# Kernel tuning notes

Measured on AMD Instinct MI355X. Metric: run time of the kernel, lower is better.

Reference implementation:

```python
import jax, jax.numpy as jnp
import numpy as np

N, E, F_IN, HID, HEADS, G = 50000, 800000, 128, 32, 8, 64
NEG_SLOPE = 0.2  # PyG GATConv default leaky_relu slope


def gat_conv(x, src, dst, W, att_src, att_dst, bias, heads, out_ch):
    """PyG-style GATConv (concat=True, self-loops already included in src/dst)."""
    n = x.shape[0]
    h = (x @ W).reshape(n, heads, out_ch)            # [N,H,C]
    a_src = jnp.sum(h * att_src, axis=-1)            # [N,H]
    a_dst = jnp.sum(h * att_dst, axis=-1)            # [N,H]
    e = jax.nn.leaky_relu(a_src[src] + a_dst[dst], NEG_SLOPE)  # [Et,H]
    # segment softmax over incoming edges of each destination node
    m = jax.ops.segment_max(e, dst, num_segments=n)
    e = jnp.exp(e - m[dst])
    denom = jax.ops.segment_sum(e, dst, num_segments=n)
    alpha = e / (denom[dst] + 1e-16)                 # [Et,H]
    msg = h[src] * alpha[:, :, None]                 # [Et,H,C]
    out = jax.ops.segment_sum(msg, dst, num_segments=n)
    return out.reshape(n, heads * out_ch) + bias


def setup_inputs() -> dict:
    key = jax.random.key(0)
    ks = jax.random.split(key, 16)
    x = jax.random.normal(ks[0], (N, F_IN), dtype=jnp.float32)
    edge_index = jax.random.randint(ks[1], (2, E), 0, N, dtype=jnp.int64)
    batch = jnp.sort(jax.random.randint(ks[2], (N,), 0, G, dtype=jnp.int64))
    s = 0.05
    params = dict(
        W1=jax.random.normal(ks[3], (F_IN, HEADS * HID), jnp.float32) * s,
        att_src1=jax.random.normal(ks[4], (1, HEADS, HID), jnp.float32) * s,
        att_dst1=jax.random.normal(ks[5], (1, HEADS, HID), jnp.float32) * s,
        b1=jnp.zeros((HEADS * HID,), jnp.float32),
        W2=jax.random.normal(ks[6], (HEADS * HID, HID), jnp.float32) * s,
        att_src2=jax.random.normal(ks[7], (1, 1, HID), jnp.float32) * s,
        att_dst2=jax.random.normal(ks[8], (1, 1, HID), jnp.float32) * s,
        b2=jnp.zeros((HID,), jnp.float32),
        Wo=jax.random.normal(ks[9], (HID, 1), jnp.float32) * s,
        bo=jnp.zeros((1,), jnp.float32),
    )
    return dict(x=x, edge_index=edge_index, batch=batch, **params)


def reference(x, edge_index, batch, W1, att_src1, att_dst1, b1,
              W2, att_src2, att_dst2, b2, Wo, bo):
    # add self loops (PyG GATConv default add_self_loops=True)
    loop = jnp.arange(N, dtype=edge_index.dtype)
    src = jnp.concatenate([edge_index[0], loop])
    dst = jnp.concatenate([edge_index[1], loop])

    h = jax.nn.elu(gat_conv(x, src, dst, W1, att_src1, att_dst1, b1, HEADS, HID))
    # dropout p=0.2 is identity in eval mode
    h = jax.nn.elu(gat_conv(h, src, dst, W2, att_src2, att_dst2, b2, 1, HID))

    # global mean pool over graphs
    sums = jax.ops.segment_sum(h, batch, num_segments=G)          # [G,HID]
    cnts = jax.ops.segment_sum(jnp.ones((N,), h.dtype), batch, num_segments=G)
    pooled = sums / jnp.maximum(cnts, 1.0)[:, None]

    return jax.nn.sigmoid(pooled @ Wo + bo)                        # [G,1]
```

## Files before the change

### kernel.cpp

```cpp
#include <hip/hip_runtime.h>
#include <hip/hip_bf16.h>
#include <math.h>

#define NN 50000
#define NE 800000
#define ET (NE + NN)
#define FIN 128
#define HEADS 8
#define HID 32
#define C1 (HEADS * HID)
#define NG 64
#define NEG 0.2f

#define EPB 4096
#define NBKT 782
#define CAP 2048

typedef __attribute__((ext_vector_type(8))) unsigned short ushort8_t;
typedef __attribute__((ext_vector_type(4))) unsigned short ushort4_t;
typedef __attribute__((ext_vector_type(2))) float float2_t;
typedef __attribute__((ext_vector_type(8))) short bf16x8;
typedef __attribute__((ext_vector_type(4))) float f32x4;

__device__ __forceinline__ float lrelu(float v) { return v > 0.f ? v : NEG * v; }
__device__ __forceinline__ float elu1(float v)  { return v > 0.f ? v : expm1f(v); }
__device__ __forceinline__ unsigned short f2bf(float f) {
    __hip_bfloat16 b = __float2bfloat16(f);
    return *reinterpret_cast<unsigned short*>(&b);
}
__device__ __forceinline__ float bf2f(unsigned short u) {
    return __uint_as_float(((unsigned)u) << 16);
}
__device__ __forceinline__ void dec_fma16(uint4 r, float e, float2_t* acc) {
    float2_t ev = {e, e};
    acc[0] += ev * __builtin_amdgcn_cvt_pk_f32_fp8((int)r.x, false);
    acc[1] += ev * __builtin_amdgcn_cvt_pk_f32_fp8((int)r.x, true);
    acc[2] += ev * __builtin_amdgcn_cvt_pk_f32_fp8((int)r.y, false);
    acc[3] += ev * __builtin_amdgcn_cvt_pk_f32_fp8((int)r.y, true);
    acc[4] += ev * __builtin_amdgcn_cvt_pk_f32_fp8((int)r.z, false);
    acc[5] += ev * __builtin_amdgcn_cvt_pk_f32_fp8((int)r.z, true);
    acc[6] += ev * __builtin_amdgcn_cvt_pk_f32_fp8((int)r.w, false);
    acc[7] += ev * __builtin_amdgcn_cvt_pk_f32_fp8((int)r.w, true);
}

__global__ __launch_bounds__(256) void bkt_scatter_kernel(const int* __restrict__ ei,
                                                          int* __restrict__ bcur,
                                                          unsigned* __restrict__ bkt) {
    __shared__ unsigned ep[EPB];
    __shared__ int lh[NBKT];
    int t = threadIdx.x;
    int base = blockIdx.x * EPB;
    int nloc = ET - base; if (nloc > EPB) nloc = EPB;
    for (int i = t; i < NBKT; i += 256) lh[i] = 0;
    __syncthreads();
    for (int k = t; k < nloc; k += 256) {
        int i = base + k;
        int s, d;
        if (i < NE) { s = ei[i]; d = ei[NE + i]; }
        else        { s = i - NE; d = s; }
        ep[k] = (unsigned)s | ((unsigned)(d & 63) << 16) | ((unsigned)(d >> 6) << 22);
        atomicAdd(&lh[d >> 6], 1);
    }
    __syncthreads();
    for (int i = t; i < NBKT; i += 256) {
        int c = lh[i];
        lh[i] = c ? atomicAdd(&bcur[i], c) : 0;
    }
    __syncthreads();
    for (int k = t; k < nloc; k += 256) {
        unsigned v = ep[k];
        int b = (int)(v >> 22);
        int pos = atomicAdd(&lh[b], 1);
        if (pos < CAP) bkt[(size_t)b * CAP + pos] = v & 0x3FFFFFu;
    }
}

__global__ __launch_bounds__(256) void bkt_scan_kernel(const int* __restrict__ bcur,
                                                       int* __restrict__ bbase,
                                                       int* __restrict__ rowptr) {
    __shared__ int wsum[4];
    int t = threadIdx.x, lane = t & 63, w = t >> 6;
    int idx = t * 4;
    int a0 = (idx + 0 < NBKT) ? bcur[idx + 0] : 0;
    int a1 = (idx + 1 < NBKT) ? bcur[idx + 1] : 0;
    int a2 = (idx + 2 < NBKT) ? bcur[idx + 2] : 0;
    int a3 = (idx + 3 < NBKT) ? bcur[idx + 3] : 0;
    int v = a0 + a1 + a2 + a3;
    int inc = v;
    #pragma unroll
    for (int off = 1; off < 64; off <<= 1) {
        int u = __shfl_up(inc, off, 64);
        if (lane >= off) inc += u;
    }
    if (lane == 63) wsum[w] = inc;
    __syncthreads();
    int woff = 0;
    #pragma unroll
    for (int i = 0; i < 4; ++i) if (i < w) woff += wsum[i];
    int excl = woff + inc - v;
    if (idx + 0 < NBKT) bbase[idx + 0] = excl;
    if (idx + 1 < NBKT) bbase[idx + 1] = excl + a0;
    if (idx + 2 < NBKT) bbase[idx + 2] = excl + a0 + a1;
    if (idx + 3 < NBKT) bbase[idx + 3] = excl + a0 + a1 + a2;
    if (t == 255) rowptr[NN] = woff + inc;
}

__global__ __launch_bounds__(256) void csr_kernel(const unsigned* __restrict__ bkt,
                                                  const int* __restrict__ bcur,
                                                  const int* __restrict__ bbase,
                                                  int* __restrict__ rowptr,
                                                  int* __restrict__ ssrc) {
    __shared__ int nb[64];
    __shared__ int nc[64];
    int b = blockIdx.x, t = threadIdx.x;
    int cnt = bcur[b]; if (cnt > CAP) cnt = CAP;
    int gbase = bbase[b];
    if (t < 64) nc[t] = 0;
    __syncthreads();
    const unsigned* e = bkt + (size_t)b * CAP;
    for (int k = t; k < cnt; k += 256)
        atomicAdd(&nc[e[k] >> 16], 1);
    __syncthreads();
    if (t < 64) {
        int v = nc[t];
        int inc = v;
        #pragma unroll
        for (int off = 1; off < 64; off <<= 1) {
            int u = __shfl_up(inc, off, 64);
            if (t >= off) inc += u;
        }
        int start = gbase + inc - v;
        nb[t] = start;
        int node = b * 64 + t;
        if (node < NN) rowptr[node] = start;
    }
    __syncthreads();
    for (int k = t; k < cnt; k += 256) {
        unsigned v = e[k];
        int pos = atomicAdd(&nb[v >> 16], 1);
        ssrc[pos] = (int)(v & 0xFFFFu);
    }
}

__global__ __launch_bounds__(256) void cvt_w1_kernel(const float* __restrict__ W1,
                                                     unsigned short* __restrict__ w1swz) {
    int t = blockIdx.x * 256 + threadIdx.x;
    int fid = t >> 6, lane = t & 63;
    int tnt = fid >> 2, ks = fid & 3;
    int n = tnt * 16 + (lane & 15);
    int k0 = ks * 32 + (lane >> 4) * 8;
    ushort8_t o;
    #pragma unroll
    for (int j = 0; j < 8; ++j) o[j] = f2bf(W1[(k0 + j) * C1 + n]);
    *(ushort8_t*)&w1swz[(size_t)(fid * 64 + lane) * 8] = o;
}

__global__ __launch_bounds__(256) void cvt_w2_kernel(const float* __restrict__ W2,
                                                     unsigned short* __restrict__ w2swz) {
    int t = blockIdx.x * 256 + threadIdx.x;
    int fid = t >> 6, lane = t & 63;
    int nt = fid >> 3, ks = fid & 7;
    int n = nt * 16 + (lane & 15);
    int k0 = ks * 32 + (lane >> 4) * 8;
    ushort8_t o;
    #pragma unroll
    for (int j = 0; j < 8; ++j) o[j] = f2bf(W2[(k0 + j) * HID + n]);
    *(ushort8_t*)&w2swz[(size_t)(fid * 64 + lane) * 8] = o;
}

__global__ __launch_bounds__(256) void gemm1_kernel(
        const float* __restrict__ x, const unsigned short* __restrict__ w1swz,
        const float* __restrict__ attS, const float* __restrict__ attD,
        unsigned char* __restrict__ h1f8, float* __restrict__ aS, float* __restrict__ aD) {
    __shared__ float lds[4 * 16 * 132];
    int t = threadIdx.x, w = t >> 6, lane = t & 63;
    int mh = w & 1, nh = w >> 1;
    int m0 = blockIdx.x * 64 + mh * 32;
    int l15 = lane & 15, l4 = lane >> 4;

    f32x4 acc[2][8];
    #pragma unroll
    for (int mt = 0; mt < 2; ++mt)
        #pragma unroll
        for (int nt = 0; nt < 8; ++nt)
            acc[mt][nt] = (f32x4){0.f, 0.f, 0.f, 0.f};

    int ra = m0 + l15;       if (ra >= NN) ra = NN - 1;
    int rb = m0 + 16 + l15;  if (rb >= NN) rb = NN - 1;
    const float* a0p = x + (size_t)ra * FIN + l4 * 8;
    const float* a1p = x + (size_t)rb * FIN + l4 * 8;

    #pragma unroll
    for (int ks = 0; ks < 4; ++ks) {
        float4 f00 = *(const float4*)(a0p + ks * 32);
        float4 f01 = *(const float4*)(a0p + ks * 32 + 4);
        float4 f10 = *(const float4*)(a1p + ks * 32);
        float4 f11 = *(const float4*)(a1p + ks * 32 + 4);
        bf16x8 af0, af1;
        af0[0] = (short)f2bf(f00.x); af0[1] = (short)f2bf(f00.y);
        af0[2] = (short)f2bf(f00.z); af0[3] = (short)f2bf(f00.w);
        af0[4] = (short)f2bf(f01.x); af0[5] = (short)f2bf(f01.y);
        af0[6] = (short)f2bf(f01.z); af0[7] = (short)f2bf(f01.w);
        af1[0] = (short)f2bf(f10.x); af1[1] = (short)f2bf(f10.y);
        af1[2] = (short)f2bf(f10.z); af1[3] = (short)f2bf(f10.w);
        af1[4] = (short)f2bf(f11.x); af1[5] = (short)f2bf(f11.y);
        af1[6] = (short)f2bf(f11.z); af1[7] = (short)f2bf(f11.w);
        #pragma unroll
        for (int nt = 0; nt < 8; ++nt) {
            bf16x8 bf = *(const bf16x8*)&w1swz[(size_t)(((nh * 8 + nt) * 4 + ks) * 64 + lane) * 8];
            acc[0][nt] = __builtin_amdgcn_mfma_f32_16x16x32_bf16(af0, bf, acc[0][nt], 0, 0, 0);
            acc[1][nt] = __builtin_amdgcn_mfma_f32_16x16x32_bf16(af1, bf, acc[1][nt], 0, 0, 0);
        }
    }

    float* wl = lds + w * 16 * 132;
    #pragma unroll
    for (int mt = 0; mt < 2; ++mt) {
        __syncthreads();
        #pragma unroll
        for (int nt = 0; nt < 8; ++nt)
            #pragma unroll
            for (int r = 0; r < 4; ++r)
                wl[(l4 * 4 + r) * 132 + nt * 16 + l15] = acc[mt][nt][r];
        __syncthreads();
        int row_g = m0 + mt * 16 + l15;
        int cch = l4;
        float v[32];
        #pragma unroll
        for (int i = 0; i < 8; ++i) {
            float4 f = *(const float4*)&wl[l15 * 132 + cch * 32 + i * 4];
            v[i * 4 + 0] = f.x; v[i * 4 + 1] = f.y; v[i * 4 + 2] = f.z; v[i * 4 + 3] = f.w;
        }
        if (row_g < NN) {
            unsigned pk[8];
            #pragma unroll
            for (int i = 0; i < 8; ++i) {
                int p = __builtin_amdgcn_cvt_pk_fp8_f32(v[i * 4 + 0], v[i * 4 + 1], 0, false);
                p = __builtin_amdgcn_cvt_pk_fp8_f32(v[i * 4 + 2], v[i * 4 + 3], p, true);
                pk[i] = (unsigned)p;
            }
            size_t base = (size_t)row_g * C1 + nh * 128 + cch * 32;
            *(uint4*)&h1f8[base]      = make_uint4(pk[0], pk[1], pk[2], pk[3]);
            *(uint4*)&h1f8[base + 16] = make_uint4(pk[4], pk[5], pk[6], pk[7]);
            int h = nh * 4 + cch;
            float ps = 0.f, pd = 0.f;
            #pragma unroll
            for (int i = 0; i < 32; ++i) {
                ps += v[i] * attS[h * 32 + i];
                pd += v[i] * attD[h * 32 + i];
            }
            aS[row_g * HEADS + h] = ps;
            aD[row_g * HEADS + h] = pd;
        }
    }
}

__global__ __launch_bounds__(256) void agg1_kernel(
        const int* __restrict__ rowptr, const int* __restrict__ ssrc,
        const float* __restrict__ aS, const float* __restrict__ aD,
        const unsigned char* __restrict__ h1f8, const float* __restrict__ b1,
        unsigned short* __restrict__ z1b) {
    int d = (blockIdx.x * 256 + threadIdx.x) >> 6;
    int lane = threadIdx.x & 63;
    if (d >= NN) return;
    int start = rowptr[d], end = rowptr[d + 1];
    int q = lane >> 4, sl = lane & 15;
    int h = sl >> 1;
    float adh = aD[d * HEADS + h];
    float2_t acc[8];
    #pragma unroll
    for (int i = 0; i < 8; ++i) acc[i] = (float2_t){0.f, 0.f};
    float den = 0.f;
    int j = start + q;
    for (; j + 4 < end; j += 8) {
        int s0 = ssrc[j], s1 = ssrc[j + 4];
        uint4 r0 = *(const uint4*)&h1f8[(size_t)s0 * C1 + sl * 16];
        uint4 r1 = *(const uint4*)&h1f8[(size_t)s1 * C1 + sl * 16];
        float e0 = __expf(lrelu(aS[s0 * HEADS + h] + adh));
        float e1 = __expf(lrelu(aS[s1 * HEADS + h] + adh));
        den += e0 + e1;
        dec_fma16(r0, e0, acc);
        dec_fma16(r1, e1, acc);
    }
    for (; j < end; j += 4) {
        int s = ssrc[j];
        uint4 r = *(const uint4*)&h1f8[(size_t)s * C1 + sl * 16];
        float e = __expf(lrelu(aS[s * HEADS + h] + adh));
        den += e;
        dec_fma16(r, e, acc);
    }
    den += __shfl_xor(den, 16, 64);
    den += __shfl_xor(den, 32, 64);
    #pragma unroll
    for (int i = 0; i < 8; ++i) {
        acc[i].x += __shfl_xor(acc[i].x, 16, 64);
        acc[i].y += __shfl_xor(acc[i].y, 16, 64);
        acc[i].x += __shfl_xor(acc[i].x, 32, 64);
        acc[i].y += __shfl_xor(acc[i].y, 32, 64);
    }
    float invd = 1.f / (den + 1e-16f);
    int cb = sl * 16 + q * 4;
    float4 bb = *(const float4*)&b1[cb];
    ushort4_t o;
    o[0] = f2bf(elu1(acc[q * 2 + 0].x * invd + bb.x));
    o[1] = f2bf(elu1(acc[q * 2 + 0].y * invd + bb.y));
    o[2] = f2bf(elu1(acc[q * 2 + 1].x * invd + bb.z));
    o[3] = f2bf(elu1(acc[q * 2 + 1].y * invd + bb.w));
    *(ushort4_t*)&z1b[(size_t)d * C1 + cb] = o;
}

__global__ __launch_bounds__(256) void gemm2_kernel(
        const unsigned short* __restrict__ z1b, const unsigned short* __restrict__ w2swz,
        const float* __restrict__ attS, const float* __restrict__ attD,
        unsigned short* __restrict__ h2b, float* __restrict__ aS2, float* __restrict__ aD2) {
    __shared__ float lds[4 * 16 * 36];
    int t = threadIdx.x, w = t >> 6, lane = t & 63;
    int m0 = blockIdx.x * 64 + w * 16;
    int l15 = lane & 15, l4 = lane >> 4;

    f32x4 acc[2];
    acc[0] = (f32x4){0.f, 0.f, 0.f, 0.f};
    acc[1] = (f32x4){0.f, 0.f, 0.f, 0.f};

    int ra = m0 + l15; if (ra >= NN) ra = NN - 1;
    const unsigned short* ap = z1b + (size_t)ra * C1 + l4 * 8;

    #pragma unroll
    for (int ks = 0; ks < 8; ++ks) {
        bf16x8 af = *(const bf16x8*)(ap + ks * 32);
        #pragma unroll
        for (int nt = 0; nt < 2; ++nt) {
            bf16x8 bf = *(const bf16x8*)&w2swz[(size_t)((nt * 8 + ks) * 64 + lane) * 8];
            acc[nt] = __builtin_amdgcn_mfma_f32_16x16x32_bf16(af, bf, acc[nt], 0, 0, 0);
        }
    }
    float* wl = lds + w * 16 * 36;
    #pragma unroll
    for (int nt = 0; nt < 2; ++nt)
        #pragma unroll
        for (int r = 0; r < 4; ++r)
            wl[(l4 * 4 + r) * 36 + nt * 16 + l15] = acc[nt][r];
    __syncthreads();
    int row_g = m0 + l15;
    float v[8];
    {
        float4 f0 = *(const float4*)&wl[l15 * 36 + l4 * 8];
        float4 f1 = *(const float4*)&wl[l15 * 36 + l4 * 8 + 4];
        v[0] = f0.x; v[1] = f0.y; v[2] = f0.z; v[3] = f0.w;
        v[4] = f1.x; v[5] = f1.y; v[6] = f1.z; v[7] = f1.w;
    }
    float ps = 0.f, pd = 0.f;
    #pragma unroll
    for (int i = 0; i < 8; ++i) {
        ps += v[i] * attS[l4 * 8 + i];
        pd += v[i] * attD[l4 * 8 + i];
    }
    ps += __shfl_xor(ps, 16, 64); ps += __shfl_xor(ps, 32, 64);
    pd += __shfl_xor(pd, 16, 64); pd += __shfl_xor(pd, 32, 64);
    if (row_g < NN) {
        ushort8_t o;
        #pragma unroll
        for (int i = 0; i < 8; ++i) o[i] = f2bf(v[i]);
        *(ushort8_t*)&h2b[(size_t)row_g * HID + l4 * 8] = o;
        if (l4 == 0) { aS2[row_g] = ps; aD2[row_g] = pd; }
    }
}

__global__ __launch_bounds__(256) void agg2_kernel(
        const int* __restrict__ rowptr, const int* __restrict__ ssrc,
        const float* __restrict__ aS, const float* __restrict__ aD,
        const unsigned short* __restrict__ h2b, const float* __restrict__ b2,
        float* __restrict__ z2) {
    int d = (blockIdx.x * 256 + threadIdx.x) >> 6;
    int lane = threadIdx.x & 63;
    if (d >= NN) return;
    int start = rowptr[d], end = rowptr[d + 1];
    int q = lane >> 4, sl = lane & 15;
    float adv = aD[d];
    float2_t a = {0.f, 0.f};
    float den = 0.f;
    int j = start + q;
    for (; j + 4 < end; j += 8) {
        int s0 = ssrc[j], s1 = ssrc[j + 4];
        unsigned r0 = *(const unsigned*)&h2b[(size_t)s0 * HID + sl * 2];
        unsigned r1 = *(const unsigned*)&h2b[(size_t)s1 * HID + sl * 2];
        float e0 = __expf(lrelu(aS[s0] + adv));
        float e1 = __expf(lrelu(aS[s1] + adv));
        den += e0 + e1;
        float2_t v0 = {bf2f((unsigned short)(r0 & 0xffff)), bf2f((unsigned short)(r0 >> 16))};
        float2_t v1 = {bf2f((unsigned short)(r1 & 0xffff)), bf2f((unsigned short)(r1 >> 16))};
        a += (float2_t){e0, e0} * v0;
        a += (float2_t){e1, e1} * v1;
    }
    for (; j < end; j += 4) {
        int s = ssrc[j];
        unsigned r = *(const unsigned*)&h2b[(size_t)s * HID + sl * 2];
        float e = __expf(lrelu(aS[s] + adv));
        den += e;
        float2_t v = {bf2f((unsigned short)(r & 0xffff)), bf2f((unsigned short)(r >> 16))};
        a += (float2_t){e, e} * v;
    }
    den += __shfl_xor(den, 16, 64);
    den += __shfl_xor(den, 32, 64);
    a.x += __shfl_xor(a.x, 16, 64); a.x += __shfl_xor(a.x, 32, 64);
    a.y += __shfl_xor(a.y, 16, 64); a.y += __shfl_xor(a.y, 32, 64);
    if (q == 0) {
        float invd = 1.f / (den + 1e-16f);
        float2 o;
        o.x = elu1(a.x * invd + b2[sl * 2]);
        o.y = elu1(a.y * invd + b2[sl * 2 + 1]);
        *(float2*)&z2[(size_t)d * HID + sl * 2] = o;
    }
}

__global__ __launch_bounds__(256) void pool_partial_kernel(
        const float* __restrict__ z2, const int* __restrict__ batch,
        float* __restrict__ pooled) {
    __shared__ float sm[256];
    int g = blockIdx.x >> 4, slice = blockIdx.x & 15;
    int t = threadIdx.x;
    int lo = 0, hi = NN;
    while (lo < hi) { int m = (lo + hi) >> 1; if (batch[m] < g) lo = m + 1; else hi = m; }
    int start = lo;
    hi = NN;
    while (lo < hi) { int m = (lo + hi) >> 1; if (batch[m] < g + 1) lo = m + 1; else hi = m; }
    int end = lo;
    int len = end - start;
    int s0 = start + (int)(((long long)len * slice) >> 4);
    int s1 = start + (int)(((long long)len * (slice + 1)) >> 4);
    int c = t & 31, r = t >> 5;
    float acc = 0.f;
    for (int n = s0 + r; n < s1; n += 8)
        acc += z2[(size_t)n * HID + c];
    sm[t] = acc;
    __syncthreads();
    if (t < 32) {
        float s = 0.f;
        #pragma unroll
        for (int i = 0; i < 8; ++i) s += sm[t + 32 * i];
        atomicAdd(&pooled[g * HID + t], s);
    }
}

__global__ void pool_finish_kernel(const float* __restrict__ pooled,
                                   const int* __restrict__ batch,
                                   const float* __restrict__ Wo, const float* __restrict__ bo,
                                   float* __restrict__ out) {
    int g = threadIdx.x;
    if (g >= NG) return;
    int lo = 0, hi = NN;
    while (lo < hi) { int m = (lo + hi) >> 1; if (batch[m] < g) lo = m + 1; else hi = m; }
    int start = lo;
    hi = NN;
    while (lo < hi) { int m = (lo + hi) >> 1; if (batch[m] < g + 1) lo = m + 1; else hi = m; }
    int end = lo;
    float c = fmaxf((float)(end - start), 1.f);
    float acc = 0.f;
    for (int i = 0; i < HID; ++i) acc += (pooled[g * HID + i] / c) * Wo[i];
    acc += bo[0];
    out[g] = 1.f / (1.f + __expf(-acc));
}

extern "C" void kernel_launch(void* const* d_in, const int* in_sizes, int n_in,
                              void* d_out, int out_size, void* d_ws, size_t ws_size,
                              hipStream_t stream) {
    const float* x     = (const float*)d_in[0];
    const int*   ei    = (const int*)d_in[1];
    const int*   batch = (const int*)d_in[2];
    const float* W1    = (const float*)d_in[3];
    const float* attS1 = (const float*)d_in[4];
    const float* attD1 = (const float*)d_in[5];
    const float* b1    = (const float*)d_in[6];
    const float* W2    = (const float*)d_in[7];
    const float* attS2 = (const float*)d_in[8];
    const float* attD2 = (const float*)d_in[9];
    const float* b2    = (const float*)d_in[10];
    const float* Wo    = (const float*)d_in[11];
    const float* bo    = (const float*)d_in[12];
    float* out = (float*)d_out;

    char* p = (char*)d_ws;
    auto alloc = [&](size_t bytes) {
        char* r = p;
        p += (bytes + 255) & ~(size_t)255;
        return (void*)r;
    };
    unsigned char*  h1f8  = (unsigned char*)alloc((size_t)NN * C1);
    unsigned short* w1swz = (unsigned short*)alloc((size_t)FIN * C1 * 2);
    unsigned short* w2swz = (unsigned short*)alloc((size_t)C1 * HID * 2);
    unsigned short* z1b   = (unsigned short*)alloc((size_t)NN * C1 * 2);
    unsigned short* h2b   = (unsigned short*)alloc((size_t)NN * HID * 2);
    float* aS1    = (float*)alloc((size_t)NN * HEADS * 4);
    float* aD1    = (float*)alloc((size_t)NN * HEADS * 4);
    float* z2     = (float*)alloc((size_t)NN * HID * 4);
    float* aS2    = (float*)alloc((size_t)NN * 4);
    float* aD2    = (float*)alloc((size_t)NN * 4);
    int*   rowptr = (int*)alloc((size_t)(NN + 1) * 4);
    int*   ssrc   = (int*)alloc((size_t)ET * 4);
    unsigned* bkt = (unsigned*)alloc((size_t)NBKT * CAP * 4);
    int*   bbase  = (int*)alloc((size_t)NBKT * 4);
    int*   bcur   = (int*)alloc((size_t)NBKT * 4);
    float* pooled = (float*)alloc((size_t)NG * HID * 4);
    size_t zero_bytes = (size_t)(p - (char*)bcur);

    hipMemsetAsync(bcur, 0, zero_bytes, stream);
    bkt_scatter_kernel<<<(ET + EPB - 1) / EPB, 256, 0, stream>>>(ei, bcur, bkt);
    bkt_scan_kernel<<<1, 256, 0, stream>>>(bcur, bbase, rowptr);
    csr_kernel<<<NBKT, 256, 0, stream>>>(bkt, bcur, bbase, rowptr, ssrc);
    cvt_w1_kernel<<<16, 256, 0, stream>>>(W1, w1swz);
    cvt_w2_kernel<<<4, 256, 0, stream>>>(W2, w2swz);
    gemm1_kernel<<<(NN + 63) / 64, 256, 0, stream>>>(x, w1swz, attS1, attD1, h1f8, aS1, aD1);
    agg1_kernel<<<(NN * 64) / 256, 256, 0, stream>>>(rowptr, ssrc, aS1, aD1, h1f8, b1, z1b);
    gemm2_kernel<<<(NN + 63) / 64, 256, 0, stream>>>(z1b, w2swz, attS2, attD2, h2b, aS2, aD2);
    agg2_kernel<<<(NN * 64 + 255) / 256, 256, 0, stream>>>(rowptr, ssrc, aS2, aD2, h2b, b2, z2);
    pool_partial_kernel<<<NG * 16, 256, 0, stream>>>(z2, batch, pooled);
    pool_finish_kernel<<<1, 64, 0, stream>>>(pooled, batch, Wo, bo, out);
}
```

Measured before the change: 244.0 us.

## Cut kernel launches by fusing scan, weight conversion and pooling; unroll aggregation loops

Removes the single-block bucket scan by having each CSR block compute its own base offset as a reduction over preceding bucket counts. It also merges the two weight conversion kernels into one launch, and merges the pool partial and finish kernels into one block per graph, which removes the atomics and the pooled buffer. The aggregation loops in both GAT layers now process four edges per iteration instead of two, to expose more memory-level parallelism. The trade-offs are redundant prefix reads in csr_kernel, which grow with block index, and only 64 blocks doing the pooling.

Result: slower. 271.8 us (+11.4%).

```diff
diff --git a/kernel.cpp b/kernel.cpp
--- a/kernel.cpp
+++ b/kernel.cpp
@@ -75,48 +75,30 @@
     }
 }
 
-__global__ __launch_bounds__(256) void bkt_scan_kernel(const int* __restrict__ bcur,
-                                                       int* __restrict__ bbase,
-                                                       int* __restrict__ rowptr) {
-    __shared__ int wsum[4];
-    int t = threadIdx.x, lane = t & 63, w = t >> 6;
-    int idx = t * 4;
-    int a0 = (idx + 0 < NBKT) ? bcur[idx + 0] : 0;
-    int a1 = (idx + 1 < NBKT) ? bcur[idx + 1] : 0;
-    int a2 = (idx + 2 < NBKT) ? bcur[idx + 2] : 0;
-    int a3 = (idx + 3 < NBKT) ? bcur[idx + 3] : 0;
-    int v = a0 + a1 + a2 + a3;
-    int inc = v;
-    #pragma unroll
-    for (int off = 1; off < 64; off <<= 1) {
-        int u = __shfl_up(inc, off, 64);
-        if (lane >= off) inc += u;
-    }
-    if (lane == 63) wsum[w] = inc;
-    __syncthreads();
-    int woff = 0;
-    #pragma unroll
-    for (int i = 0; i < 4; ++i) if (i < w) woff += wsum[i];
-    int excl = woff + inc - v;
-    if (idx + 0 < NBKT) bbase[idx + 0] = excl;
-    if (idx + 1 < NBKT) bbase[idx + 1] = excl + a0;
-    if (idx + 2 < NBKT) bbase[idx + 2] = excl + a0 + a1;
-    if (idx + 3 < NBKT) bbase[idx + 3] = excl + a0 + a1 + a2;
-    if (t == 255) rowptr[NN] = woff + inc;
-}
-
 __global__ __launch_bounds__(256) void csr_kernel(const unsigned* __restrict__ bkt,
                                                   const int* __restrict__ bcur,
-                                                  const int* __restrict__ bbase,
                                                   int* __restrict__ rowptr,
                                                   int* __restrict__ ssrc) {
     __shared__ int nb[64];
     __shared__ int nc[64];
+    __shared__ int red[256];
     int b = blockIdx.x, t = threadIdx.x;
+    int partial = 0;
+    for (int i = t; i < b; i += 256) partial += bcur[i];
+    red[t] = partial;
+    if (t < 64) nc[t] = 0;
+    __syncthreads();
+    if (t < 128) red[t] += red[t + 128];
+    __syncthreads();
+    if (t < 64) {
+        int v = red[t] + red[t + 64];
+        #pragma unroll
+        for (int off = 32; off; off >>= 1) v += __shfl_down(v, off, 64);
+        if (t == 0) red[0] = v;
+    }
+    __syncthreads();
+    int gbase = red[0];
     int cnt = bcur[b]; if (cnt > CAP) cnt = CAP;
-    int gbase = bbase[b];
-    if (t < 64) nc[t] = 0;
-    __syncthreads();
     const unsigned* e = bkt + (size_t)b * CAP;
     for (int k = t; k < cnt; k += 256)
         atomicAdd(&nc[e[k] >> 16], 1);
@@ -134,6 +116,7 @@
         int node = b * 64 + t;
         if (node < NN) rowptr[node] = start;
     }
+    if (b == NBKT - 1 && t == 0) rowptr[NN] = gbase + cnt;
     __syncthreads();
     for (int k = t; k < cnt; k += 256) {
         unsigned v = e[k];
@@ -142,30 +125,32 @@
     }
 }
 
-__global__ __launch_bounds__(256) void cvt_w1_kernel(const float* __restrict__ W1,
-                                                     unsigned short* __restrict__ w1swz) {
-    int t = blockIdx.x * 256 + threadIdx.x;
-    int fid = t >> 6, lane = t & 63;
-    int tnt = fid >> 2, ks = fid & 3;
-    int n = tnt * 16 + (lane & 15);
-    int k0 = ks * 32 + (lane >> 4) * 8;
-    ushort8_t o;
-    #pragma unroll
-    for (int j = 0; j < 8; ++j) o[j] = f2bf(W1[(k0 + j) * C1 + n]);
-    *(ushort8_t*)&w1swz[(size_t)(fid * 64 + lane) * 8] = o;
-}
-
-__global__ __launch_bounds__(256) void cvt_w2_kernel(const float* __restrict__ W2,
-                                                     unsigned short* __restrict__ w2swz) {
-    int t = blockIdx.x * 256 + threadIdx.x;
-    int fid = t >> 6, lane = t & 63;
-    int nt = fid >> 3, ks = fid & 7;
-    int n = nt * 16 + (lane & 15);
-    int k0 = ks * 32 + (lane >> 4) * 8;
-    ushort8_t o;
-    #pragma unroll
-    for (int j = 0; j < 8; ++j) o[j] = f2bf(W2[(k0 + j) * HID + n]);
-    *(ushort8_t*)&w2swz[(size_t)(fid * 64 + lane) * 8] = o;
+__global__ __launch_bounds__(256) void cvt_w_kernel(const float* __restrict__ W1,
+                                                    const float* __restrict__ W2,
+                                                    unsigned short* __restrict__ w1swz,
+                                                    unsigned short* __restrict__ w2swz) {
+    int bid = blockIdx.x;
+    if (bid < 16) {
+        int t = bid * 256 + threadIdx.x;
+        int fid = t >> 6, lane = t & 63;
+        int tnt = fid >> 2, ks = fid & 3;
+        int n = tnt * 16 + (lane & 15);
+        int k0 = ks * 32 + (lane >> 4) * 8;
+        ushort8_t o;
+        #pragma unroll
+        for (int j = 0; j < 8; ++j) o[j] = f2bf(W1[(k0 + j) * C1 + n]);
+        *(ushort8_t*)&w1swz[(size_t)(fid * 64 + lane) * 8] = o;
+    } else {
+        int t = (bid - 16) * 256 + threadIdx.x;
+        int fid = t >> 6, lane = t & 63;
+        int nt = fid >> 3, ks = fid & 7;
+        int n = nt * 16 + (lane & 15);
+        int k0 = ks * 32 + (lane >> 4) * 8;
+        ushort8_t o;
+        #pragma unroll
+        for (int j = 0; j < 8; ++j) o[j] = f2bf(W2[(k0 + j) * HID + n]);
+        *(ushort8_t*)&w2swz[(size_t)(fid * 64 + lane) * 8] = o;
+    }
 }
 
 __global__ __launch_bounds__(256) void gemm1_kernel(
@@ -272,15 +257,21 @@
     for (int i = 0; i < 8; ++i) acc[i] = (float2_t){0.f, 0.f};
     float den = 0.f;
     int j = start + q;
-    for (; j + 4 < end; j += 8) {
-        int s0 = ssrc[j], s1 = ssrc[j + 4];
+    for (; j + 12 < end; j += 16) {
+        int s0 = ssrc[j], s1 = ssrc[j + 4], s2 = ssrc[j + 8], s3 = ssrc[j + 12];
         uint4 r0 = *(const uint4*)&h1f8[(size_t)s0 * C1 + sl * 16];
         uint4 r1 = *(const uint4*)&h1f8[(size_t)s1 * C1 + sl * 16];
+        uint4 r2 = *(const uint4*)&h1f8[(size_t)s2 * C1 + sl * 16];
+        uint4 r3 = *(const uint4*)&h1f8[(size_t)s3 * C1 + sl * 16];
         float e0 = __expf(lrelu(aS[s0 * HEADS + h] + adh));
         float e1 = __expf(lrelu(aS[s1 * HEADS + h] + adh));
-        den += e0 + e1;
+        float e2 = __expf(lrelu(aS[s2 * HEADS + h] + adh));
+        float e3 = __expf(lrelu(aS[s3 * HEADS + h] + adh));
+        den += e0 + e1 + e2 + e3;
         dec_fma16(r0, e0, acc);
         dec_fma16(r1, e1, acc);
+        dec_fma16(r2, e2, acc);
+        dec_fma16(r3, e3, acc);
     }
     for (; j < end; j += 4) {
         int s = ssrc[j];
@@ -380,25 +371,28 @@
     float2_t a = {0.f, 0.f};
     float den = 0.f;
     int j = start + q;
-    for (; j + 4 < end; j += 8) {
-        int s0 = ssrc[j], s1 = ssrc[j + 4];
+    for (; j + 12 < end; j += 16) {
+        int s0 = ssrc[j], s1 = ssrc[j + 4], s2 = ssrc[j + 8], s3 = ssrc[j + 12];
         unsigned r0 = *(const unsigned*)&h2b[(size_t)s0 * HID + sl * 2];
         unsigned r1 = *(const unsigned*)&h2b[(size_t)s1 * HID + sl * 2];
+        unsigned r2 = *(const unsigned*)&h2b[(size_t)s2 * HID + sl * 2];
+        unsigned r3 = *(const unsigned*)&h2b[(size_t)s3 * HID + sl * 2];
         float e0 = __expf(lrelu(aS[s0] + adv));
         float e1 = __expf(lrelu(aS[s1] + adv));
-        den += e0 + e1;
-        float2_t v0 = {bf2f((unsigned short)(r0 & 0xffff)), bf2f((unsigned short)(r0 >> 16))};
-        float2_t v1 = {bf2f((unsigned short)(r1 & 0xffff)), bf2f((unsigned short)(r1 >> 16))};
-        a += (float2_t){e0, e0} * v0;
-        a += (float2_t){e1, e1} * v1;
+        float e2 = __expf(lrelu(aS[s2] + adv));
+        float e3 = __expf(lrelu(aS[s3] + adv));
+        den += e0 + e1 + e2 + e3;
+        a += (float2_t){e0, e0} * (float2_t){bf2f((unsigned short)(r0 & 0xffff)), bf2f((unsigned short)(r0 >> 16))};
+        a += (float2_t){e1, e1} * (float2_t){bf2f((unsigned short)(r1 & 0xffff)), bf2f((unsigned short)(r1 >> 16))};
+        a += (float2_t){e2, e2} * (float2_t){bf2f((unsigned short)(r2 & 0xffff)), bf2f((unsigned short)(r2 >> 16))};
+        a += (float2_t){e3, e3} * (float2_t){bf2f((unsigned short)(r3 & 0xffff)), bf2f((unsigned short)(r3 >> 16))};
     }
     for (; j < end; j += 4) {
         int s = ssrc[j];
         unsigned r = *(const unsigned*)&h2b[(size_t)s * HID + sl * 2];
         float e = __expf(lrelu(aS[s] + adv));
         den += e;
-        float2_t v = {bf2f((unsigned short)(r & 0xffff)), bf2f((unsigned short)(r >> 16))};
-        a += (float2_t){e, e} * v;
+        a += (float2_t){e, e} * (float2_t){bf2f((unsigned short)(r & 0xffff)), bf2f((unsigned short)(r >> 16))};
     }
     den += __shfl_xor(den, 16, 64);
     den += __shfl_xor(den, 32, 64);
@@ -413,11 +407,12 @@
     }
 }
 
-__global__ __launch_bounds__(256) void pool_partial_kernel(
+__global__ __launch_bounds__(256) void pool_kernel(
         const float* __restrict__ z2, const int* __restrict__ batch,
-        float* __restrict__ pooled) {
+        const float* __restrict__ Wo, const float* __restrict__ bo,
+        float* __restrict__ out) {
     __shared__ float sm[256];
-    int g = blockIdx.x >> 4, slice = blockIdx.x & 15;
+    int g = blockIdx.x;
     int t = threadIdx.x;
     int lo = 0, hi = NN;
     while (lo < hi) { int m = (lo + hi) >> 1; if (batch[m] < g) lo = m + 1; else hi = m; }
@@ -425,12 +420,9 @@
     hi = NN;
     while (lo < hi) { int m = (lo + hi) >> 1; if (batch[m] < g + 1) lo = m + 1; else hi = m; }
     int end = lo;
-    int len = end - start;
-    int s0 = start + (int)(((long long)len * slice) >> 4);
-    int s1 = start + (int)(((long long)len * (slice + 1)) >> 4);
     int c = t & 31, r = t >> 5;
     float acc = 0.f;
-    for (int n = s0 + r; n < s1; n += 8)
+    for (int n = start + r; n < end; n += 8)
         acc += z2[(size_t)n * HID + c];
     sm[t] = acc;
     __syncthreads();
@@ -438,27 +430,12 @@
         float s = 0.f;
         #pragma unroll
         for (int i = 0; i < 8; ++i) s += sm[t + 32 * i];
-        atomicAdd(&pooled[g * HID + t], s);
-    }
-}
-
-__global__ void pool_finish_kernel(const float* __restrict__ pooled,
-                                   const int* __restrict__ batch,
-                                   const float* __restrict__ Wo, const float* __restrict__ bo,
-                                   float* __restrict__ out) {
-    int g = threadIdx.x;
-    if (g >= NG) return;
-    int lo = 0, hi = NN;
-    while (lo < hi) { int m = (lo + hi) >> 1; if (batch[m] < g) lo = m + 1; else hi = m; }
-    int start = lo;
-    hi = NN;
-    while (lo < hi) { int m = (lo + hi) >> 1; if (batch[m] < g + 1) lo = m + 1; else hi = m; }
-    int end = lo;
-    float c = fmaxf((float)(end - start), 1.f);
-    float acc = 0.f;
-    for (int i = 0; i < HID; ++i) acc += (pooled[g * HID + i] / c) * Wo[i];
-    acc += bo[0];
-    out[g] = 1.f / (1.f + __expf(-acc));
+        float cntf = fmaxf((float)(end - start), 1.f);
+        float part = (s / cntf) * Wo[t];
+        #pragma unroll
+        for (int off = 16; off; off >>= 1) part += __shfl_xor(part, off, 32);
+        if (t == 0) out[g] = 1.f / (1.f + __expf(-(part + bo[0])));
+    }
 }
 
 extern "C" void kernel_launch(void* const* d_in, const int* in_sizes, int n_in,
@@ -498,21 +475,15 @@
     int*   rowptr = (int*)alloc((size_t)(NN + 1) * 4);
     int*   ssrc   = (int*)alloc((size_t)ET * 4);
     unsigned* bkt = (unsigned*)alloc((size_t)NBKT * CAP * 4);
-    int*   bbase  = (int*)alloc((size_t)NBKT * 4);
     int*   bcur   = (int*)alloc((size_t)NBKT * 4);
-    float* pooled = (float*)alloc((size_t)NG * HID * 4);
-    size_t zero_bytes = (size_t)(p - (char*)bcur);
-
-    hipMemsetAsync(bcur, 0, zero_bytes, stream);
+
+    hipMemsetAsync(bcur, 0, (size_t)NBKT * 4, stream);
     bkt_scatter_kernel<<<(ET + EPB - 1) / EPB, 256, 0, stream>>>(ei, bcur, bkt);
-    bkt_scan_kernel<<<1, 256, 0, stream>>>(bcur, bbase, rowptr);
-    csr_kernel<<<NBKT, 256, 0, stream>>>(bkt, bcur, bbase, rowptr, ssrc);
-    cvt_w1_kernel<<<16, 256, 0, stream>>>(W1, w1swz);
-    cvt_w2_kernel<<<4, 256, 0, stream>>>(W2, w2swz);
+    csr_kernel<<<NBKT, 256, 0, stream>>>(bkt, bcur, rowptr, ssrc);
+    cvt_w_kernel<<<20, 256, 0, stream>>>(W1, W2, w1swz, w2swz);
     gemm1_kernel<<<(NN + 63) / 64, 256, 0, stream>>>(x, w1swz, attS1, attD1, h1f8, aS1, aD1);
     agg1_kernel<<<(NN * 64) / 256, 256, 0, stream>>>(rowptr, ssrc, aS1, aD1, h1f8, b1, z1b);
     gemm2_kernel<<<(NN + 63) / 64, 256, 0, stream>>>(z1b, w2swz, attS2, attD2, h2b, aS2, aD2);
     agg2_kernel<<<(NN * 64 + 255) / 256, 256, 0, stream>>>(rowptr, ssrc, aS2, aD2, h2b, b2, z2);
-    pool_partial_kernel<<<NG * 16, 256, 0, stream>>>(z2, batch, pooled);
-    pool_finish_kernel<<<1, 64, 0, stream>>>(pooled, batch, Wo, bo, out);
-}
+    pool_kernel<<<NG, 256, 0, stream>>>(z2, batch, Wo, bo, out);
+}
```
